# Performance work log

Hardware: AMD Instinct MI355X
Metric: run time of the kernel (lower is better)

Reference implementation:

```python
import jax, jax.numpy as jnp
import numpy as np
from jax import lax

DN = ('NCHW', 'OIHW', 'NCHW')

def _conv(x, w, pad):
    return lax.conv_general_dilated(x, w, (1, 1), pad, dimension_numbers=DN)

def _bn(x, p, eps=1e-5):
    # p: [4, C] rows = gamma, beta, mean, var ; inference-mode batchnorm
    g, b, m, v = p[0], p[1], p[2], p[3]
    scale = g / jnp.sqrt(v + eps)
    return (x - m[:, None, None]) * scale[:, None, None] + b[:, None, None]

def setup_inputs() -> dict:
    key = jax.random.key(0)
    ks = jax.random.split(key, 12)
    B, C, H, W = 16, 512, 56, 56
    mid = C // 2
    def bn_params(k):
        k1, k2, k3, k4 = jax.random.split(k, 4)
        g = 1.0 + 0.1 * jax.random.normal(k1, (mid,), jnp.float32)
        b = 0.1 * jax.random.normal(k2, (mid,), jnp.float32)
        m = 0.1 * jax.random.normal(k3, (mid,), jnp.float32)
        v = 0.5 + jax.random.uniform(k4, (mid,), jnp.float32)
        return jnp.stack([g, b, m, v])
    return {
        'x': jax.random.normal(ks[0], (B, C, H, W), jnp.float32),
        'w_main': 0.03 * jax.random.normal(ks[1], (mid, C, 3, 3), jnp.float32),
        'w_1x1': 0.05 * jax.random.normal(ks[2], (mid, C, 1, 1), jnp.float32),
        'w31': 0.05 * jax.random.normal(ks[3], (mid, C, 1, 1), jnp.float32),
        'bn31': bn_params(ks[4]),
        'w33': 0.05 * jax.random.normal(ks[5], (mid, mid, 3, 3), jnp.float32),
        'bn33': bn_params(ks[6]),
        'wa1': 0.05 * jax.random.normal(ks[7], (mid, C, 1, 1), jnp.float32),
        'bna1': bn_params(ks[8]),
        'bna2': bn_params(ks[9]),
        'fuse_weight': jnp.ones((4,), jnp.float32),
        'c_score': jax.random.normal(ks[10], (2 * C,), jnp.float32),
    }

def reference(x, w_main, w_1x1, w31, bn31, w33, bn33, wa1, bna1, bna2, fuse_weight, c_score):
    c = x.shape[1]
    # four branches (note: forward applies BN only inside the 3x3 and avg branches)
    acs_main = _conv(x * fuse_weight[0], w_main, 'SAME')
    acs_1x1 = _conv(x * fuse_weight[1], w_1x1, 'VALID')
    acs_3x3 = _bn(_conv(_bn(_conv(x * fuse_weight[2], w31, 'VALID'), bn31), w33, 'SAME'), bn33)
    avg_in = _bn(_conv(x * fuse_weight[3], wa1, 'VALID'), bna1)
    # AvgPool2d(k=3, s=1, p=1, count_include_pad=True)
    pooled = lax.reduce_window(avg_in, 0.0, lax.add, (1, 1, 3, 3), (1, 1, 1, 1),
                               [(0, 0), (0, 0), (1, 1), (1, 1)]) / 9.0
    acs_avg = _bn(pooled, bna2)
    out = jnp.concatenate([acs_main, acs_1x1, acs_3x3, acs_avg], axis=1)  # [B, 2c, H, W]
    # sparse 1x1 selection: output channel i = input channel ind[i] * sigmoid(c_score[ind[i]])
    _, ind = lax.top_k(c_score, c)
    scale = jax.nn.sigmoid(c_score)[ind]  # [c]
    out = out[:, ind] * scale[None, :, None, None]
    return out
```

## Files before the change

### kernel.cpp

```cpp
#include <hip/hip_runtime.h>
#include <hip/hip_bf16.h>
#include <cstdint>
#include <cstddef>

typedef _Float16 f16x8_t __attribute__((ext_vector_type(8)));
typedef float    f32x4_t __attribute__((ext_vector_type(4)));
typedef unsigned short u16x8_t __attribute__((ext_vector_type(8)));
typedef unsigned short u16x4_t __attribute__((ext_vector_type(4)));

__device__ __forceinline__ unsigned short f2h(float f) {
    return __builtin_bit_cast(unsigned short, (_Float16)f);
}
__device__ __forceinline__ float h2f(unsigned short h) {
    return (float)__builtin_bit_cast(_Float16, h);
}
__device__ __forceinline__ f16x8_t load_h8(const unsigned short* p) {
    u16x8_t r = *(const u16x8_t*)p;
    return __builtin_bit_cast(f16x8_t, r);
}

#define BATCH 16
#define CFULL 512
#define CMID  256
#define HW    3136
#define WDIM  56

#define POS_STRIDE_SH 40
#define LDS_SHORTS (348 * 40)

__global__ void prep_tabs(const float* __restrict__ cscore,
                          const float* __restrict__ bn31, const float* __restrict__ bn33,
                          const float* __restrict__ bna1, const float* __restrict__ bna2,
                          int* __restrict__ pos_tab, float* __restrict__ scale_tab,
                          float* __restrict__ bnab)
{
    __shared__ float s[1024];
    int t = threadIdx.x;
    s[t] = cscore[t];
    __syncthreads();
    float sj = s[t];
    int cnt = 0;
    for (int k = 0; k < 1024; ++k) {
        float sk = s[k];
        cnt += (sk > sj) || (sk == sj && k < t);
    }
    pos_tab[t]   = (cnt < 512) ? cnt : -1;
    scale_tab[t] = 1.0f / (1.0f + expf(-sj));

    if (t < 256) {
        const float* srcs[4] = {bn31, bn33, bna1, bna2};
        #pragma unroll
        for (int q = 0; q < 4; ++q) {
            const float* sp = srcs[q];
            float g = sp[t], b = sp[256 + t], m = sp[512 + t], v = sp[768 + t];
            float a = g * rsqrtf(v + 1e-5f);
            bnab[q * 512 + t]       = a;
            bnab[q * 512 + 256 + t] = b - m * a;
        }
    }
}

__global__ void prep_weights(const float* __restrict__ w_main, const float* __restrict__ w_1x1,
                             const float* __restrict__ w31, const float* __restrict__ wa1,
                             const float* __restrict__ w33, const float* __restrict__ fw,
                             unsigned short* __restrict__ Wcat,
                             unsigned short* __restrict__ Wmain,
                             unsigned short* __restrict__ W33r)
{
    int i = blockIdx.x * 256 + threadIdx.x;
    if (i < 393216) {
        int row = i >> 9, c = i & 511;
        float v;
        if (row < 256)      v = w_1x1[row * 512 + c] * fw[1];
        else if (row < 512) v = w31[(row - 256) * 512 + c] * fw[2];
        else                v = wa1[(row - 512) * 512 + c] * fw[3];
        Wcat[((c >> 5) * 768 + row) * 32 + (c & 31)] = f2h(v);
    } else if (i < 393216 + 1179648) {
        int j = i - 393216;
        int o = j / 4608, r = j % 4608, tap = r >> 9, c = r & 511;
        Wmain[(((c >> 5) * 9 + tap) * 256 + o) * 32 + (c & 31)] =
            f2h(w_main[(size_t)(o * 512 + c) * 9 + tap] * fw[0]);
    } else if (i < 2162688) {
        int j = i - 1572864;
        int o = j / 2304, r = j % 2304, tap = r >> 8, c = r & 255;
        W33r[(((c >> 5) * 9 + tap) * 256 + o) * 32 + (c & 31)] =
            f2h(w33[(size_t)(o * 256 + c) * 9 + tap]);
    }
}

__global__ void transpose_x(const float* __restrict__ x, unsigned short* __restrict__ xt)
{
    __shared__ unsigned short tile[64][65];
    int t = threadIdx.x;
    int hw0 = blockIdx.x * 64, c0 = blockIdx.y * 64, b = blockIdx.z;
    const float* xb = x + ((size_t)b * CFULL + c0) * HW + hw0;
    int hwL = t & 63, cL = t >> 6;
    #pragma unroll
    for (int i = 0; i < 16; ++i) {
        int c = cL + i * 4;
        tile[c][hwL] = f2h(xb[(size_t)c * HW + hwL]);
    }
    __syncthreads();
    int c8 = (t & 7) * 8, hw = t >> 3;
    #pragma unroll
    for (int i = 0; i < 2; ++i) {
        int hh = hw + i * 32;
        u16x8_t v;
        #pragma unroll
        for (int j = 0; j < 8; ++j) v[j] = tile[c8 + j][hh];
        *(u16x8_t*)(xt + ((size_t)b * HW + hw0 + hh) * CFULL + c0 + c8) = v;
    }
}

template<int CIN, int NTAP, int MODE>
__device__ __forceinline__ void conv_body(
    const unsigned short* __restrict__ X,
    const unsigned short* __restrict__ Wr,
    float* __restrict__ out,
    unsigned short* __restrict__ u_dst,
    unsigned short* __restrict__ avg_dst,
    const float* __restrict__ bnab,
    const int* __restrict__ pos_tab,
    const float* __restrict__ scale_tab,
    unsigned short* smem, int b, int ob, int pb)
{
    const int t    = threadIdx.x;
    const int lane = t & 63;
    const int wid  = t >> 6;
    const int wm = wid >> 1, wn = wid & 1;
    const int lr = lane & 15;
    const int ko = (lane >> 4) * 8;
    const int row0 = pb * 4;

    const int o_wave = ob * 128 + wm * 64;
    const int p_wave = pb * 224 + wn * 112;

    int bofs[7];
    #pragma unroll
    for (int n = 0; n < 7; ++n) {
        int p = p_wave + n * 16 + lr;
        bofs[n] = ((p / WDIM - row0) * 58 + p % WDIM) * POS_STRIDE_SH + ko;
    }

    const int r_lo = (NTAP == 9) ? 0 : 1;
    const int nitems = ((NTAP == 9) ? 6 : 4) * 224;
    int  s_src[6];
    int  s_dst[6];
    bool s_val[6];
    #pragma unroll
    for (int i = 0; i < 6; ++i) {
        int idx = t + i * 256;
        bool act = idx < nitems;
        int r   = r_lo + idx / 224;
        int rm  = idx % 224;
        int col = rm >> 2, sub = rm & 3;
        int ir  = row0 + r - 1;
        s_val[i] = act && ((unsigned)ir < (unsigned)WDIM);
        s_src[i] = (ir * WDIM + col) * CIN + sub * 8;
        s_dst[i] = (r * 58 + col + 1) * POS_STRIDE_SH + sub * 8;
    }

    #pragma unroll
    for (int i = 0; i < 7; ++i) {
        int j = t + i * 256;
        if (j < LDS_SHORTS / 8)
            *(u16x8_t*)(smem + j * 8) = (u16x8_t){0, 0, 0, 0, 0, 0, 0, 0};
    }

    f32x4_t acc[4][7];
    #pragma unroll
    for (int m = 0; m < 4; ++m)
        #pragma unroll
        for (int n = 0; n < 7; ++n)
            acc[m][n] = (f32x4_t){0.f, 0.f, 0.f, 0.f};

    const int astep = (MODE == 1) ? 768 * 32 : 256 * 32;
    const unsigned short* am[4];
    #pragma unroll
    for (int m = 0; m < 4; ++m)
        am[m] = Wr + (size_t)(o_wave + m * 16 + lr) * 32 + ko;

    const unsigned short* xb = X + (size_t)b * HW * CIN;
    const int KCH = CIN / 32;

    u16x8_t sbuf[6];
    #pragma unroll
    for (int i = 0; i < 6; ++i)
        if (s_val[i]) sbuf[i] = *(const u16x8_t*)(xb + s_src[i]);

    for (int kch = 0; kch < KCH; ++kch) {
        __syncthreads();
        #pragma unroll
        for (int i = 0; i < 6; ++i)
            if (s_val[i]) *(u16x8_t*)(smem + s_dst[i]) = sbuf[i];
        __syncthreads();

        if (kch + 1 < KCH) {
            #pragma unroll
            for (int i = 0; i < 6; ++i)
                if (s_val[i]) sbuf[i] = *(const u16x8_t*)(xb + s_src[i] + (kch + 1) * 32);
        }

        f16x8_t afn[4];
        #pragma unroll
        for (int m = 0; m < 4; ++m)
            afn[m] = load_h8(am[m] + (size_t)(kch * NTAP) * astep);

        #pragma unroll
        for (int tap = 0; tap < NTAP; ++tap) {
            f16x8_t afc[4];
            #pragma unroll
            for (int m = 0; m < 4; ++m) afc[m] = afn[m];
            if (tap + 1 < NTAP) {
                #pragma unroll
                for (int m = 0; m < 4; ++m)
                    afn[m] = load_h8(am[m] + (size_t)(kch * NTAP + tap + 1) * astep);
            }
            const int toff = (NTAP == 9) ? (((tap / 3) * 58 + tap % 3) * POS_STRIDE_SH)
                                         : (59 * POS_STRIDE_SH);
            f16x8_t bf[7];
            #pragma unroll
            for (int n = 0; n < 7; ++n)
                bf[n] = load_h8(smem + bofs[n] + toff);
            #pragma unroll
            for (int m = 0; m < 4; ++m)
                #pragma unroll
                for (int n = 0; n < 7; ++n)
                    acc[m][n] = __builtin_amdgcn_mfma_f32_16x16x32_f16(afc[m], bf[n], acc[m][n], 0, 0, 0);
        }
    }

    const int fq = lane >> 4;
    const int seg = (MODE == 1) ? (ob >> 1) : 0;
    const bool bn_write = (MODE == 1) && (seg != 0);

    #pragma unroll
    for (int m = 0; m < 4; ++m) {
        const int orow = o_wave + m * 16 + fq * 4;
        #pragma unroll
        for (int n = 0; n < 7; ++n) {
            const int p = p_wave + n * 16 + lr;
            f32x4_t v = acc[m][n];
            if (bn_write) {
                const int lc0 = orow - seg * 256;
                const float* ab = (seg == 1) ? (bnab + 0 * 512) : (bnab + 2 * 512);
                unsigned short* dst = (seg == 1) ? u_dst : avg_dst;
                u16x4_t pk;
                #pragma unroll
                for (int j = 0; j < 4; ++j) {
                    float a = ab[lc0 + j], bb = ab[256 + lc0 + j];
                    pk[j] = f2h(a * v[j] + bb);
                }
                *(u16x4_t*)(dst + ((size_t)b * HW + p) * CMID + lc0) = pk;
            } else {
                const int cbase = (MODE == 0) ? 0 : ((MODE == 2) ? 512 : 256);
                #pragma unroll
                for (int j = 0; j < 4; ++j) {
                    int o = orow + j;
                    float val2 = v[j];
                    if (MODE == 2) val2 = bnab[512 + o] * val2 + bnab[512 + 256 + o];
                    int jc = cbase + o;
                    int pos = pos_tab[jc];
                    if (pos >= 0)
                        out[((size_t)b * CFULL + pos) * HW + p] = val2 * scale_tab[jc];
                }
            }
        }
    }
}

__global__ __launch_bounds__(256, 2)
void convA(const unsigned short* __restrict__ X,
           const unsigned short* __restrict__ Wmain,
           const unsigned short* __restrict__ Wcat,
           float* __restrict__ out,
           unsigned short* __restrict__ u_dst,
           unsigned short* __restrict__ avg_dst,
           const float* __restrict__ bnab,
           const int* __restrict__ pos_tab,
           const float* __restrict__ scale_tab)
{
    __shared__ unsigned short smem[LDS_SHORTS];
    const int id = blockIdx.x;
    const int xcd = id & 7, slot = id >> 3;
    if (slot < 56) {
        const int b = xcd + 8 * (slot / 28);
        const int u = slot % 28;
        conv_body<512, 9, 0>(X, Wmain, out, nullptr, nullptr, bnab,
                             pos_tab, scale_tab, smem, b, u / 14, u % 14);
    } else {
        const int g = slot - 56;
        const int b = xcd + 8 * (g / 84);
        const int u = g % 84;
        conv_body<512, 1, 1>(X, Wcat, out, u_dst, avg_dst, bnab,
                             pos_tab, scale_tab, smem, b, u / 14, u % 14);
    }
}

__global__ __launch_bounds__(256, 2)
void convB(const unsigned short* __restrict__ U,
           const unsigned short* __restrict__ W33r,
           const unsigned short* __restrict__ avgin,
           float* __restrict__ out,
           const float* __restrict__ bnab,
           const int* __restrict__ pos_tab,
           const float* __restrict__ scale_tab)
{
    __shared__ unsigned short smem[LDS_SHORTS];
    const int id = blockIdx.x;
    const int xcd = id & 7, slot = id >> 3;
    if (slot < 56) {
        const int b = xcd + 8 * (slot / 28);
        const int u = slot % 28;
        conv_body<256, 9, 2>(U, W33r, out, nullptr, nullptr, bnab,
                             pos_tab, scale_tab, smem, b, u / 14, u % 14);
    } else {
        const int g = slot - 56;
        const int b = xcd + 8 * (g / 392);
        const int q = g % 392;
        const int t = threadIdx.x;
        const int p = q * 8 + (t >> 5);
        const int c0 = (t & 31) * 8;
        const int h = p / WDIM, w = p % WDIM;
        const float* ab2 = bnab + 3 * 512;
        float s[8];
        #pragma unroll
        for (int j = 0; j < 8; ++j) s[j] = 0.f;
        #pragma unroll
        for (int dh = -1; dh <= 1; ++dh) {
            int hh = h + dh;
            if ((unsigned)hh >= (unsigned)WDIM) continue;
            #pragma unroll
            for (int dw = -1; dw <= 1; ++dw) {
                int ww = w + dw;
                if ((unsigned)ww >= (unsigned)WDIM) continue;
                u16x8_t v = *(const u16x8_t*)(avgin + ((size_t)b * HW + hh * WDIM + ww) * CMID + c0);
                #pragma unroll
                for (int j = 0; j < 8; ++j) s[j] += h2f(v[j]);
            }
        }
        #pragma unroll
        for (int j = 0; j < 8; ++j) {
            int c = c0 + j;
            int jc = 768 + c;
            int pos = pos_tab[jc];
            if (pos >= 0) {
                float val = (s[j] * (1.f / 9.f)) * ab2[c] + ab2[256 + c];
                out[((size_t)b * CFULL + pos) * HW + p] = val * scale_tab[jc];
            }
        }
    }
}

extern "C" void kernel_launch(void* const* d_in, const int* in_sizes, int n_in,
                              void* d_out, int out_size, void* d_ws, size_t ws_size,
                              hipStream_t stream) {
    (void)in_sizes; (void)n_in; (void)out_size; (void)ws_size;
    const float* x      = (const float*)d_in[0];
    const float* w_main = (const float*)d_in[1];
    const float* w_1x1  = (const float*)d_in[2];
    const float* w31    = (const float*)d_in[3];
    const float* bn31   = (const float*)d_in[4];
    const float* w33    = (const float*)d_in[5];
    const float* bn33   = (const float*)d_in[6];
    const float* wa1    = (const float*)d_in[7];
    const float* bna1   = (const float*)d_in[8];
    const float* bna2   = (const float*)d_in[9];
    const float* fw     = (const float*)d_in[10];
    const float* cscore = (const float*)d_in[11];
    float* out = (float*)d_out;

    char* ws = (char*)d_ws;
    unsigned short* x_nhwc = (unsigned short*)(ws);
    unsigned short* u_nhwc = (unsigned short*)(ws + 51380224);
    unsigned short* avgin  = (unsigned short*)(ws + 77070336);
    unsigned short* Wcat   = (unsigned short*)(ws + 102760448);
    unsigned short* Wmain  = (unsigned short*)(ws + 103546880);
    unsigned short* W33r   = (unsigned short*)(ws + 105906176);
    float*          bnab   = (float*)        (ws + 107085824);
    int*            pos_tab= (int*)          (ws + 107094016);
    float*          scl_tab= (float*)        (ws + 107098112);

    dim3 blk(256);

    prep_tabs<<<dim3(1), dim3(1024), 0, stream>>>(cscore, bn31, bn33, bna1, bna2,
                                                  pos_tab, scl_tab, bnab);
    prep_weights<<<dim3(8448), blk, 0, stream>>>(w_main, w_1x1, w31, wa1, w33, fw,
                                                 Wcat, Wmain, W33r);
    transpose_x<<<dim3(49, 8, 16), blk, 0, stream>>>(x, x_nhwc);

    convA<<<dim3(1792), blk, 0, stream>>>(x_nhwc, Wmain, Wcat, out,
                                          u_nhwc, avgin, bnab, pos_tab, scl_tab);

    convB<<<dim3(6720), blk, 0, stream>>>(u_nhwc, W33r, avgin, out,
                                          bnab, pos_tab, scl_tab);
}
```

Before: 443.0 us.

## Double-buffer LDS input tiles and raise MFMA wave priority

The shared-memory input tile becomes double-buffered, so the next K-chunk is written to the alternate buffer while MFMAs read the current one. This removes one of the two barriers per chunk. The register prefetch of weight fragments across taps is replaced by a direct load per tap, and s_setprio is raised around the MFMA block. LDS use doubles, which may limit occupancy below two blocks per CU, and the loss of weight prefetch can expose global load latency.

Result: faster. 425.2 us (-4.0%).

```diff
diff --git a/kernel.cpp b/kernel.cpp
--- a/kernel.cpp
+++ b/kernel.cpp
@@ -161,9 +161,9 @@
     }
 
     #pragma unroll
-    for (int i = 0; i < 7; ++i) {
+    for (int i = 0; i < 14; ++i) {
         int j = t + i * 256;
-        if (j < LDS_SHORTS / 8)
+        if (j < 2 * LDS_SHORTS / 8)
             *(u16x8_t*)(smem + j * 8) = (u16x8_t){0, 0, 0, 0, 0, 0, 0, 0};
     }
 
@@ -187,47 +187,53 @@
     #pragma unroll
     for (int i = 0; i < 6; ++i)
         if (s_val[i]) sbuf[i] = *(const u16x8_t*)(xb + s_src[i]);
+    __syncthreads();
+    #pragma unroll
+    for (int i = 0; i < 6; ++i)
+        if (s_val[i]) *(u16x8_t*)(smem + s_dst[i]) = sbuf[i];
+    if (KCH > 1) {
+        #pragma unroll
+        for (int i = 0; i < 6; ++i)
+            if (s_val[i]) sbuf[i] = *(const u16x8_t*)(xb + s_src[i] + 32);
+    }
+    __syncthreads();
 
     for (int kch = 0; kch < KCH; ++kch) {
-        __syncthreads();
-        #pragma unroll
-        for (int i = 0; i < 6; ++i)
-            if (s_val[i]) *(u16x8_t*)(smem + s_dst[i]) = sbuf[i];
-        __syncthreads();
+        unsigned short* wbuf = smem + ((kch + 1) & 1) * LDS_SHORTS;
+        const unsigned short* rbuf = smem + (kch & 1) * LDS_SHORTS;
 
         if (kch + 1 < KCH) {
             #pragma unroll
             for (int i = 0; i < 6; ++i)
-                if (s_val[i]) sbuf[i] = *(const u16x8_t*)(xb + s_src[i] + (kch + 1) * 32);
-        }
-
-        f16x8_t afn[4];
-        #pragma unroll
-        for (int m = 0; m < 4; ++m)
-            afn[m] = load_h8(am[m] + (size_t)(kch * NTAP) * astep);
+                if (s_val[i]) *(u16x8_t*)(wbuf + s_dst[i]) = sbuf[i];
+        }
+        if (kch + 2 < KCH) {
+            #pragma unroll
+            for (int i = 0; i < 6; ++i)
+                if (s_val[i]) sbuf[i] = *(const u16x8_t*)(xb + s_src[i] + (kch + 2) * 32);
+        }
 
         #pragma unroll
         for (int tap = 0; tap < NTAP; ++tap) {
-            f16x8_t afc[4];
-            #pragma unroll
-            for (int m = 0; m < 4; ++m) afc[m] = afn[m];
-            if (tap + 1 < NTAP) {
-                #pragma unroll
-                for (int m = 0; m < 4; ++m)
-                    afn[m] = load_h8(am[m] + (size_t)(kch * NTAP + tap + 1) * astep);
-            }
             const int toff = (NTAP == 9) ? (((tap / 3) * 58 + tap % 3) * POS_STRIDE_SH)
                                          : (59 * POS_STRIDE_SH);
+            f16x8_t af[4];
+            #pragma unroll
+            for (int m = 0; m < 4; ++m)
+                af[m] = load_h8(am[m] + (size_t)(kch * NTAP + tap) * astep);
             f16x8_t bf[7];
             #pragma unroll
             for (int n = 0; n < 7; ++n)
-                bf[n] = load_h8(smem + bofs[n] + toff);
+                bf[n] = load_h8(rbuf + bofs[n] + toff);
+            __builtin_amdgcn_s_setprio(1);
             #pragma unroll
             for (int m = 0; m < 4; ++m)
                 #pragma unroll
                 for (int n = 0; n < 7; ++n)
-                    acc[m][n] = __builtin_amdgcn_mfma_f32_16x16x32_f16(afc[m], bf[n], acc[m][n], 0, 0, 0);
-        }
+                    acc[m][n] = __builtin_amdgcn_mfma_f32_16x16x32_f16(af[m], bf[n], acc[m][n], 0, 0, 0);
+            __builtin_amdgcn_s_setprio(0);
+        }
+        __syncthreads();
     }
 
     const int fq = lane >> 4;
@@ -280,7 +286,7 @@
            const int* __restrict__ pos_tab,
            const float* __restrict__ scale_tab)
 {
-    __shared__ unsigned short smem[LDS_SHORTS];
+    __shared__ unsigned short smem[2 * LDS_SHORTS];
     const int id = blockIdx.x;
     const int xcd = id & 7, slot = id >> 3;
     if (slot < 56) {
@@ -306,7 +312,7 @@
            const int* __restrict__ pos_tab,
            const float* __restrict__ scale_tab)
 {
-    __shared__ unsigned short smem[LDS_SHORTS];
+    __shared__ unsigned short smem[2 * LDS_SHORTS];
     const int id = blockIdx.x;
     const int xcd = id & 7, slot = id >> 3;
     if (slot < 56) {
```

## Rebalance conv kernels: move main 3x3 into second launch, drop prefetch, add setprio

Applied to the files above, without the earlier changes.

The main 3x3 conv over x moves out of the first launch and is interleaved with the 3x3 conv over u in the second launch. The first launch now runs only the concatenated 1x1 convs, so the long 3x3 blocks are paired and scheduled together. The inner loop drops its register double-buffering of global loads for both the activations and the weights. It loads them directly each step and raises wave priority around the MFMA block. This lowers register pressure and balances work across the two launches, at the cost of exposing global load latency.

Result: no change. 435.9 us (-1.6%).

```diff
diff --git a/kernel.cpp b/kernel.cpp
--- a/kernel.cpp
+++ b/kernel.cpp
@@ -183,50 +183,36 @@
     const unsigned short* xb = X + (size_t)b * HW * CIN;
     const int KCH = CIN / 32;
 
-    u16x8_t sbuf[6];
-    #pragma unroll
-    for (int i = 0; i < 6; ++i)
-        if (s_val[i]) sbuf[i] = *(const u16x8_t*)(xb + s_src[i]);
-
     for (int kch = 0; kch < KCH; ++kch) {
         __syncthreads();
+        u16x8_t buf[6];
         #pragma unroll
         for (int i = 0; i < 6; ++i)
-            if (s_val[i]) *(u16x8_t*)(smem + s_dst[i]) = sbuf[i];
+            if (s_val[i]) buf[i] = *(const u16x8_t*)(xb + s_src[i] + kch * 32);
+        #pragma unroll
+        for (int i = 0; i < 6; ++i)
+            if (s_val[i]) *(u16x8_t*)(smem + s_dst[i]) = buf[i];
         __syncthreads();
 
-        if (kch + 1 < KCH) {
-            #pragma unroll
-            for (int i = 0; i < 6; ++i)
-                if (s_val[i]) sbuf[i] = *(const u16x8_t*)(xb + s_src[i] + (kch + 1) * 32);
-        }
-
-        f16x8_t afn[4];
-        #pragma unroll
-        for (int m = 0; m < 4; ++m)
-            afn[m] = load_h8(am[m] + (size_t)(kch * NTAP) * astep);
-
         #pragma unroll
         for (int tap = 0; tap < NTAP; ++tap) {
-            f16x8_t afc[4];
-            #pragma unroll
-            for (int m = 0; m < 4; ++m) afc[m] = afn[m];
-            if (tap + 1 < NTAP) {
-                #pragma unroll
-                for (int m = 0; m < 4; ++m)
-                    afn[m] = load_h8(am[m] + (size_t)(kch * NTAP + tap + 1) * astep);
-            }
             const int toff = (NTAP == 9) ? (((tap / 3) * 58 + tap % 3) * POS_STRIDE_SH)
                                          : (59 * POS_STRIDE_SH);
+            f16x8_t af[4];
+            #pragma unroll
+            for (int m = 0; m < 4; ++m)
+                af[m] = load_h8(am[m] + (size_t)(kch * NTAP + tap) * astep);
             f16x8_t bf[7];
             #pragma unroll
             for (int n = 0; n < 7; ++n)
                 bf[n] = load_h8(smem + bofs[n] + toff);
+            __builtin_amdgcn_s_setprio(1);
             #pragma unroll
             for (int m = 0; m < 4; ++m)
                 #pragma unroll
                 for (int n = 0; n < 7; ++n)
-                    acc[m][n] = __builtin_amdgcn_mfma_f32_16x16x32_f16(afc[m], bf[n], acc[m][n], 0, 0, 0);
+                    acc[m][n] = __builtin_amdgcn_mfma_f32_16x16x32_f16(af[m], bf[n], acc[m][n], 0, 0, 0);
+            __builtin_amdgcn_s_setprio(0);
         }
     }
 
@@ -270,35 +256,28 @@
 }
 
 __global__ __launch_bounds__(256, 2)
-void convA(const unsigned short* __restrict__ X,
-           const unsigned short* __restrict__ Wmain,
-           const unsigned short* __restrict__ Wcat,
-           float* __restrict__ out,
-           unsigned short* __restrict__ u_dst,
-           unsigned short* __restrict__ avg_dst,
-           const float* __restrict__ bnab,
-           const int* __restrict__ pos_tab,
-           const float* __restrict__ scale_tab)
+void fusedK(const unsigned short* __restrict__ X,
+            const unsigned short* __restrict__ Wcat,
+            float* __restrict__ out,
+            unsigned short* __restrict__ u_dst,
+            unsigned short* __restrict__ avg_dst,
+            const float* __restrict__ bnab,
+            const int* __restrict__ pos_tab,
+            const float* __restrict__ scale_tab)
 {
     __shared__ unsigned short smem[LDS_SHORTS];
     const int id = blockIdx.x;
     const int xcd = id & 7, slot = id >> 3;
-    if (slot < 56) {
-        const int b = xcd + 8 * (slot / 28);
-        const int u = slot % 28;
-        conv_body<512, 9, 0>(X, Wmain, out, nullptr, nullptr, bnab,
-                             pos_tab, scale_tab, smem, b, u / 14, u % 14);
-    } else {
-        const int g = slot - 56;
-        const int b = xcd + 8 * (g / 84);
-        const int u = g % 84;
-        conv_body<512, 1, 1>(X, Wcat, out, u_dst, avg_dst, bnab,
-                             pos_tab, scale_tab, smem, b, u / 14, u % 14);
-    }
+    const int b = xcd + 8 * (slot / 84);
+    const int u = slot % 84;
+    conv_body<512, 1, 1>(X, Wcat, out, u_dst, avg_dst, bnab,
+                         pos_tab, scale_tab, smem, b, u / 14, u % 14);
 }
 
 __global__ __launch_bounds__(256, 2)
-void convB(const unsigned short* __restrict__ U,
+void longK(const unsigned short* __restrict__ X,
+           const unsigned short* __restrict__ Wmain,
+           const unsigned short* __restrict__ U,
            const unsigned short* __restrict__ W33r,
            const unsigned short* __restrict__ avgin,
            float* __restrict__ out,
@@ -309,15 +288,21 @@
     __shared__ unsigned short smem[LDS_SHORTS];
     const int id = blockIdx.x;
     const int xcd = id & 7, slot = id >> 3;
-    if (slot < 56) {
-        const int b = xcd + 8 * (slot / 28);
-        const int u = slot % 28;
-        conv_body<256, 9, 2>(U, W33r, out, nullptr, nullptr, bnab,
-                             pos_tab, scale_tab, smem, b, u / 14, u % 14);
+    if (slot < 112) {
+        const int b = xcd + 8 * (slot / 56);
+        const int rr = slot % 56;
+        const int idx = rr >> 1;
+        const int ob = idx / 14, pb = idx % 14;
+        if ((rr & 1) == 0)
+            conv_body<512, 9, 0>(X, Wmain, out, nullptr, nullptr, bnab,
+                                 pos_tab, scale_tab, smem, b, ob, pb);
+        else
+            conv_body<256, 9, 2>(U, W33r, out, nullptr, nullptr, bnab,
+                                 pos_tab, scale_tab, smem, b, ob, pb);
     } else {
-        const int g = slot - 56;
-        const int b = xcd + 8 * (g / 392);
-        const int q = g % 392;
+        const int s2 = slot - 112;
+        const int b = xcd + 8 * (s2 / 392);
+        const int q = s2 % 392;
         const int t = threadIdx.x;
         const int p = q * 8 + (t >> 5);
         const int c0 = (t & 31) * 8;
@@ -389,9 +374,9 @@
                                                  Wcat, Wmain, W33r);
     transpose_x<<<dim3(49, 8, 16), blk, 0, stream>>>(x, x_nhwc);
 
-    convA<<<dim3(1792), blk, 0, stream>>>(x_nhwc, Wmain, Wcat, out,
-                                          u_nhwc, avgin, bnab, pos_tab, scl_tab);
-
-    convB<<<dim3(6720), blk, 0, stream>>>(u_nhwc, W33r, avgin, out,
-                                          bnab, pos_tab, scl_tab);
-}
+    fusedK<<<dim3(1344), blk, 0, stream>>>(x_nhwc, Wcat, out,
+                                           u_nhwc, avgin, bnab, pos_tab, scl_tab);
+
+    longK<<<dim3(7168), blk, 0, stream>>>(x_nhwc, Wmain, u_nhwc, W33r, avgin,
+                                          out, bnab, pos_tab, scl_tab);
+}
```
